# Kernel optimization log

Hardware: AMD Instinct MI355X
Metric: run time of the kernel (lower is better)

Reference implementation:

```python
import jax, jax.numpy as jnp
import numpy as np

EMB = 1024
HEAD = 64

def setup_inputs() -> dict:
    key = jax.random.key(0)
    ks = jax.random.split(key, 7)
    s = 1.0 / np.sqrt(EMB)
    X = jax.random.normal(ks[0], (4, 4096, EMB), dtype=jnp.float32)
    Wk = jax.random.uniform(ks[1], (EMB, HEAD), jnp.float32, -s, s)
    bk = jax.random.uniform(ks[2], (HEAD,), jnp.float32, -s, s)
    Wq = jax.random.uniform(ks[3], (EMB, HEAD), jnp.float32, -s, s)
    bq = jax.random.uniform(ks[4], (HEAD,), jnp.float32, -s, s)
    Wv = jax.random.uniform(ks[5], (EMB, HEAD), jnp.float32, -s, s)
    bv = jax.random.uniform(ks[6], (HEAD,), jnp.float32, -s, s)
    return {"X": X, "Wk": Wk, "bk": bk, "Wq": Wq, "bq": bq, "Wv": Wv, "bv": bv}

def reference(X, Wk, bk, Wq, bq, Wv, bv):
    # X: [B, S, E]; projections -> [B, S, H]
    k = X @ Wk + bk
    q = X @ Wq + bq
    v = X @ Wv + bv
    S = X.shape[1]
    scale = 1.0 / np.sqrt(HEAD).astype(np.float32)
    scores = jnp.einsum('bqh,bkh->bqk', q, k) * scale  # [B, S, S]
    causal = jnp.tril(jnp.ones((S, S), dtype=bool))
    scores = jnp.where(causal, scores, -jnp.inf)
    probs = jax.nn.softmax(scores, axis=-1)
    return jnp.einsum('bqk,bkh->bqh', probs, v)
```

## Files before the change

### kernel.cpp

```cpp
#include <hip/hip_runtime.h>

#define S_LEN 4096
#define EMBD  1024
#define HEADD 64

typedef __bf16 bf16x8 __attribute__((ext_vector_type(8)));
typedef float  f32x4  __attribute__((ext_vector_type(4)));

__device__ __forceinline__ unsigned short f2bf(float f) {
  union { float f; unsigned u; } x; x.f = f;
  unsigned r = x.u + 0x7FFFu + ((x.u >> 16) & 1u);
  return (unsigned short)(r >> 16);
}

__device__ __forceinline__ bf16x8 cvt8(f32x4 a, f32x4 b) {
  union { bf16x8 v; unsigned short s[8]; } u;
#pragma unroll
  for (int j = 0; j < 4; j++) { u.s[j] = f2bf(a[j]); u.s[4 + j] = f2bf(b[j]); }
  return u.v;
}

__device__ __forceinline__ unsigned fbits(float f) {
  union { float f; unsigned u; } x; x.f = f; return x.u;
}

__global__ void prep_w(const float* __restrict__ Wk, const float* __restrict__ bk,
                       const float* __restrict__ Wq, const float* __restrict__ bq,
                       const float* __restrict__ Wv, const float* __restrict__ bv,
                       unsigned short* __restrict__ wt, float* __restrict__ bias) {
  int n = blockIdx.x;
  int t = threadIdx.x;
  const float QSCALE = 0.125f * 1.44269504088896340736f;
  const float* W; const float* bsrc; int col; float s = 1.0f;
  if (n < 64)       { W = Wk; bsrc = bk; col = n; }
  else if (n < 128) { W = Wq; bsrc = bq; col = n - 64; s = QSCALE; }
  else              { W = Wv; bsrc = bv; col = n - 128; }
  for (int k = t; k < EMBD; k += 256)
    wt[n * EMBD + k] = f2bf(W[k * HEADD + col] * s);
  if (t == 0) bias[n] = bsrc[col] * s;
}

__global__ __launch_bounds__(256, 1) void proj_qkv(
    const float* __restrict__ X, const unsigned short* __restrict__ wt,
    const float* __restrict__ bias,
    unsigned short* __restrict__ qws, unsigned short* __restrict__ kws,
    unsigned short* __restrict__ vtws) {
  __shared__ unsigned short xs[64 * 256];

  const int tid = threadIdx.x;
  const int w = tid >> 6;
  const int lane = tid & 63;
  const int l15 = lane & 15, lg = lane >> 4;
  const int row0 = blockIdx.x * 64;

  const int sr = tid >> 5;
  const int sc = (tid & 31) * 8;

  const unsigned short* wp = wt + (size_t)(w * 48 + l15) * EMBD + lg * 8;

  f32x4 acc[4][3];
#pragma unroll
  for (int g = 0; g < 4; g++)
#pragma unroll
    for (int j = 0; j < 3; j++) acc[g][j] = (f32x4){0.f, 0.f, 0.f, 0.f};

  f32x4 la[8], lb[8];
#pragma unroll
  for (int it = 0; it < 8; it++) {
    const float* src = X + (size_t)(row0 + it * 8 + sr) * EMBD + sc;
    la[it] = *(const f32x4*)src;
    lb[it] = *(const f32x4*)(src + 4);
  }
#pragma unroll
  for (int it = 0; it < 8; it++) {
    const int r = it * 8 + sr;
    int soff = (r << 8) + sc;
    soff ^= (r & 7) << 3;
    *(bf16x8*)&xs[soff] = cvt8(la[it], lb[it]);
  }
  __syncthreads();

#pragma unroll
  for (int kc = 0; kc < 4; kc++) {
    if (kc + 1 < 4) {
#pragma unroll
      for (int it = 0; it < 8; it++) {
        const float* src = X + (size_t)(row0 + it * 8 + sr) * EMBD + (kc + 1) * 256 + sc;
        la[it] = *(const f32x4*)src;
        lb[it] = *(const f32x4*)(src + 4);
      }
    }
    bf16x8 wf[2][3];
#pragma unroll
    for (int j = 0; j < 3; j++)
      wf[0][j] = *(const bf16x8*)(wp + (size_t)j * 16 * EMBD + kc * 256);
#pragma unroll
    for (int ss = 0; ss < 8; ss++) {
      const int cur = ss & 1;
      if (ss + 1 < 8) {
#pragma unroll
        for (int j = 0; j < 3; j++)
          wf[cur ^ 1][j] = *(const bf16x8*)(wp + (size_t)j * 16 * EMBD + kc * 256 + (ss + 1) * 32);
      }
      const int c = ss * 32 + lg * 8;
      bf16x8 a[4];
#pragma unroll
      for (int g = 0; g < 4; g++) {
        int so = ((g * 16 + l15) << 8) + c;
        so ^= (l15 & 7) << 3;
        a[g] = *(const bf16x8*)&xs[so];
      }
#pragma unroll
      for (int j = 0; j < 3; j++)
#pragma unroll
        for (int g = 0; g < 4; g++)
          acc[g][j] = __builtin_amdgcn_mfma_f32_16x16x32_bf16(a[g], wf[cur][j], acc[g][j], 0, 0, 0);
    }
    __syncthreads();
    if (kc + 1 < 4) {
#pragma unroll
      for (int it = 0; it < 8; it++) {
        const int r = it * 8 + sr;
        int soff = (r << 8) + sc;
        soff ^= (r & 7) << 3;
        *(bf16x8*)&xs[soff] = cvt8(la[it], lb[it]);
      }
      __syncthreads();
    }
  }

#pragma unroll
  for (int g = 0; g < 4; g++) {
    const int crow0 = row0 + g * 16 + lg * 4;
#pragma unroll
    for (int j = 0; j < 3; j++) {
      const int nf = w * 3 + j;
      const int n = nf * 16 + l15;
      const float bs = bias[n];
      if (nf < 8) {
        unsigned short* dst = (nf < 4) ? kws : qws;
        const int nn = n & 63;
#pragma unroll
        for (int i = 0; i < 4; i++)
          dst[(size_t)(crow0 + i) * HEADD + nn] = f2bf(acc[g][j][i] + bs);
      } else {
        const int d = n - 128;
        const int bb = crow0 >> 12, sr2 = crow0 & 4095;
        union { unsigned long long pk; unsigned short s[4]; } u;
#pragma unroll
        for (int i = 0; i < 4; i++) u.s[i] = f2bf(acc[g][j][i] + bs);
        *(unsigned long long*)&vtws[((size_t)bb * HEADD + d) * S_LEN + sr2] = u.pk;
      }
    }
  }
}

__global__ __launch_bounds__(512, 2) void attn(
    const unsigned short* __restrict__ qws,
    const unsigned short* __restrict__ kws,
    const unsigned short* __restrict__ vtws,
    unsigned short* __restrict__ pO,
    float* __restrict__ pmv, float* __restrict__ plv) {
  __shared__ uint4 kvb[2][1024];
  __shared__ unsigned short pbl[8][16][72];

  const int tid = threadIdx.x;
  const int w = tid >> 6;
  const int lane = tid & 63;
  const int l15 = lane & 15, lg = lane >> 4;
  const int srow = tid >> 3;
  const int scol = (tid & 7) * 8;
  const int soff = ((srow * 128 + (tid & 7) * 16)) ^ ((srow & 7) << 4);

  const int id = blockIdx.x;
  const int b = id & 3;
  const int x = (id >> 2) & 15;
  const int h = id >> 6;

  const unsigned short* kb = kws + (size_t)b * S_LEN * HEADD;
  const unsigned short* vb = vtws + (size_t)b * HEADD * S_LEN;
  const unsigned short* qp = qws + (size_t)b * S_LEN * HEADD;

#define PROC(BQ0, BQ1, O, M, LL, QB, TLX, tt)                                   \
  do {                                                                          \
    f32x4 sc[4];                                                                \
    __builtin_amdgcn_s_setprio(1);                                              \
    _Pragma("unroll")                                                           \
    for (int nf = 0; nf < 4; nf++) {                                            \
      f32x4 z = (f32x4){0.f, 0.f, 0.f, 0.f};                                    \
      z = __builtin_amdgcn_mfma_f32_16x16x32_bf16(k0[nf], BQ0, z, 0, 0, 0);     \
      sc[nf] = __builtin_amdgcn_mfma_f32_16x16x32_bf16(k1[nf], BQ1, z, 0, 0, 0);\
    }                                                                           \
    __builtin_amdgcn_s_setprio(0);                                              \
    if ((tt) == (TLX)) {                                                        \
      const int qa = (QB) + l15;                                                \
      _Pragma("unroll")                                                         \
      for (int nf = 0; nf < 4; nf++)                                            \
        _Pragma("unroll")                                                       \
        for (int i = 0; i < 4; i++)                                             \
          if ((tt) * 64 + nf * 16 + lg * 4 + i > qa) sc[nf][i] = -1.0e30f;      \
    }                                                                           \
    float pm = sc[0][0];                                                        \
    _Pragma("unroll")                                                           \
    for (int nf = 0; nf < 4; nf++)                                              \
      _Pragma("unroll")                                                         \
      for (int i = 0; i < 4; i++) pm = fmaxf(pm, sc[nf][i]);                    \
    if (!__all(pm <= M + 8.0f)) {                                               \
      float mx = fmaxf(pm, __shfl_xor(pm, 16));                                 \
      mx = fmaxf(mx, __shfl_xor(mx, 32));                                       \
      const float mn = fmaxf(M, mx);                                            \
      const float al = __builtin_amdgcn_exp2f(M - mn);                          \
      M = mn;                                                                   \
      LL *= al;                                                                 \
      float alr[4];                                                             \
      _Pragma("unroll")                                                         \
      for (int i = 0; i < 4; i++) alr[i] = __shfl(al, lg * 4 + i);              \
      _Pragma("unroll")                                                         \
      for (int nd = 0; nd < 4; nd++)                                            \
        _Pragma("unroll")                                                       \
        for (int i = 0; i < 4; i++) O[nd][i] *= alr[i];                         \
    }                                                                           \
    _Pragma("unroll")                                                           \
    for (int nf = 0; nf < 4; nf++) {                                            \
      f32x4 p;                                                                  \
      _Pragma("unroll")                                                         \
      for (int i = 0; i < 4; i++) p[i] = __builtin_amdgcn_exp2f(sc[nf][i] - M); \
      LL += p[0] + p[1] + p[2] + p[3];                                          \
      unsigned lo_ = __builtin_amdgcn_perm(fbits(p[1]) + 0x8000u,               \
                                           fbits(p[0]) + 0x8000u, 0x07060302u); \
      unsigned hi_ = __builtin_amdgcn_perm(fbits(p[3]) + 0x8000u,               \
                                           fbits(p[2]) + 0x8000u, 0x07060302u); \
      uint2 pk_; pk_.x = lo_; pk_.y = hi_;                                      \
      *(uint2*)&pbl[w][l15][nf * 16 + lg * 4] = pk_;                            \
    }                                                                           \
    const bf16x8 ap0 = *(const bf16x8*)&pbl[w][l15][lg * 8];                    \
    const bf16x8 ap1 = *(const bf16x8*)&pbl[w][l15][32 + lg * 8];               \
    __builtin_amdgcn_s_setprio(1);                                              \
    _Pragma("unroll")                                                           \
    for (int nd = 0; nd < 4; nd++) {                                            \
      f32x4 oo = __builtin_amdgcn_mfma_f32_16x16x32_bf16(ap0, v0[nd], O[nd], 0, 0, 0); \
      O[nd] = __builtin_amdgcn_mfma_f32_16x16x32_bf16(ap1, v1[nd], oo, 0, 0, 0);\
    }                                                                           \
    __builtin_amdgcn_s_setprio(0);                                              \
  } while (0)

#define LOADG(tt)                                                               \
  do {                                                                          \
    kreg = *(const uint4*)(kb + ((size_t)(tt) * 64 + srow) * HEADD + scol);     \
    vreg = *(const uint4*)(vb + (size_t)srow * S_LEN + (tt) * 64 + scol);       \
  } while (0)

#define WRITEL(bf)                                                              \
  do {                                                                          \
    unsigned char* d_ = (unsigned char*)kvb[bf];                                \
    *(uint4*)&d_[soff] = kreg;                                                  \
    *(uint4*)&d_[8192 + soff] = vreg;                                           \
  } while (0)

#pragma unroll 1
  for (int ph = 0; ph < 2; ph++) {
    const int P = ph ? x : 31 - x;
    const int tlP = 2 * P + 1;
    const int tlw = 2 * P + (w >> 2);
    const int qb = P * 128 + w * 16;

    const unsigned short* qptr = qp + (size_t)(qb + l15) * HEADD + lg * 8;
    const bf16x8 bq0 = *(const bf16x8*)qptr;
    const bf16x8 bq1 = *(const bf16x8*)(qptr + 32);

    f32x4 o[4];
#pragma unroll
    for (int nd = 0; nd < 4; nd++) o[nd] = (f32x4){0.f, 0.f, 0.f, 0.f};
    float m = -3.0e38f, l = 0.f;

    int t = h;
    if (t <= tlP) {
      uint4 kreg, vreg;
      LOADG(t);
      __syncthreads();
      WRITEL(0);
      __syncthreads();
      int cur = 0;
#pragma unroll 1
      while (true) {
        const int tn = t + 8;
        const bool hn = tn <= tlP;
        if (hn) LOADG(tn);
        if (t <= tlw) {
          bf16x8 k0[4], k1[4], v0[4], v1[4];
          const unsigned char* base = (const unsigned char*)kvb[cur];
#pragma unroll
          for (int nf = 0; nf < 4; nf++) {
            const int r = nf * 16 + l15;
            const int sw = (l15 & 7) << 4;
            const int b0 = (r * 128 + lg * 16) ^ sw;
            const int b1 = (r * 128 + 64 + lg * 16) ^ sw;
            k0[nf] = *(const bf16x8*)&base[b0];
            k1[nf] = *(const bf16x8*)&base[b1];
            v0[nf] = *(const bf16x8*)&base[8192 + b0];
            v1[nf] = *(const bf16x8*)&base[8192 + b1];
          }
          PROC(bq0, bq1, o, m, l, qb, tlw, t);
        }
        if (!hn) break;
        WRITEL(cur ^ 1);
        __syncthreads();
        cur ^= 1;
        t = tn;
      }
    }

    l += __shfl_xor(l, 16);
    l += __shfl_xor(l, 32);
    const size_t pbase = (size_t)(h * 4 + b) * S_LEN + qb;
    if (lane < 16) { pmv[pbase + lane] = m; plv[pbase + lane] = l; }
#pragma unroll
    for (int nd = 0; nd < 4; nd++)
#pragma unroll
      for (int i = 0; i < 4; i++)
        pO[(pbase + lg * 4 + i) * 64 + nd * 16 + l15] = f2bf(o[nd][i]);
  }
#undef PROC
#undef LOADG
#undef WRITEL
}

__global__ __launch_bounds__(256) void merge_attn(
    const unsigned short* __restrict__ pO,
    const float* __restrict__ pmv, const float* __restrict__ plv,
    float* __restrict__ out) {
  const int row = blockIdx.x * 64 + (threadIdx.x >> 2);
  const int q = threadIdx.x & 3;
  float mh[8], lh[8];
  float M = -3.0e38f;
#pragma unroll
  for (int hh = 0; hh < 8; hh++) {
    mh[hh] = pmv[hh * 16384 + row];
    lh[hh] = plv[hh * 16384 + row];
    M = fmaxf(M, mh[hh]);
  }
  float Lt = 0.f, a[8];
#pragma unroll
  for (int hh = 0; hh < 8; hh++) {
    a[hh] = __builtin_amdgcn_exp2f(mh[hh] - M);
    Lt += a[hh] * lh[hh];
  }
  const float iL = 1.0f / Lt;
  float acc[16];
#pragma unroll
  for (int c = 0; c < 16; c++) acc[c] = 0.f;
#pragma unroll
  for (int hh = 0; hh < 8; hh++) {
    const unsigned short* src = pO + ((size_t)hh * 16384 + row) * 64 + q * 16;
    const uint4 u0 = *(const uint4*)(src);
    const uint4 u1 = *(const uint4*)(src + 8);
    const unsigned* uu0 = (const unsigned*)&u0;
    const unsigned* uu1 = (const unsigned*)&u1;
#pragma unroll
    for (int j = 0; j < 4; j++) {
      union { unsigned u; float f; } e0, e1, e2, e3;
      e0.u = uu0[j] << 16;  e1.u = uu0[j] & 0xffff0000u;
      e2.u = uu1[j] << 16;  e3.u = uu1[j] & 0xffff0000u;
      acc[j * 2 + 0] += e0.f * a[hh];
      acc[j * 2 + 1] += e1.f * a[hh];
      acc[8 + j * 2 + 0] += e2.f * a[hh];
      acc[8 + j * 2 + 1] += e3.f * a[hh];
    }
  }
  float* dst = out + (size_t)row * 64 + q * 16;
#pragma unroll
  for (int c = 0; c < 16; c++) dst[c] = acc[c] * iL;
}

extern "C" void kernel_launch(void* const* d_in, const int* in_sizes, int n_in,
                              void* d_out, int out_size, void* d_ws, size_t ws_size,
                              hipStream_t stream) {
  const float* X  = (const float*)d_in[0];
  const float* Wk = (const float*)d_in[1];
  const float* bk = (const float*)d_in[2];
  const float* Wq = (const float*)d_in[3];
  const float* bq = (const float*)d_in[4];
  const float* Wv = (const float*)d_in[5];
  const float* bv = (const float*)d_in[6];
  float* out = (float*)d_out;

  char* ws = (char*)d_ws;
  unsigned short* kws  = (unsigned short*)(ws);
  unsigned short* qws  = (unsigned short*)(ws + (2u << 20));
  unsigned short* vtws = (unsigned short*)(ws + (4u << 20));
  unsigned short* wt   = (unsigned short*)(ws + (6u << 20));
  float*          bias = (float*)(ws + (6u << 20) + (512u << 10));
  unsigned short* pO   = (unsigned short*)(ws + (8u << 20));
  float*          pmv  = (float*)(ws + (24u << 20));
  float*          plv  = (float*)(ws + (25u << 20));

  prep_w<<<dim3(192), dim3(256), 0, stream>>>(Wk, bk, Wq, bq, Wv, bv, wt, bias);
  proj_qkv<<<dim3(256), dim3(256), 0, stream>>>(X, wt, bias, qws, kws, vtws);
  attn<<<dim3(512), dim3(512), 0, stream>>>(qws, kws, vtws, pO, pmv, plv);
  merge_attn<<<dim3(256), dim3(256), 0, stream>>>(pO, pmv, plv, out);
}
```

Baseline: 66.26 us.

## Process both paired query blocks in one pass over shared K/V tiles

Replaces the two sequential phases (high and low query block) with a single loop over K/V tiles, where each staged LDS tile is consumed by both query blocks. This avoids loading the K/V tiles for the low block a second time from global memory and staging them in LDS again, and it removes one set of barriers and phase setup. The cost is double the accumulator and Q register state per thread, which can raise register pressure and lower occupancy. LDS fragments are also re-read for each block.

```diff
diff --git a/kernel.cpp b/kernel.cpp
--- a/kernel.cpp
+++ b/kernel.cpp
@@ -181,8 +181,40 @@
   const unsigned short* vb = vtws + (size_t)b * HEADD * S_LEN;
   const unsigned short* qp = qws + (size_t)b * S_LEN * HEADD;
 
-#define PROC(BQ0, BQ1, O, M, LL, QB, TLX, tt)                                   \
+  const int PH = 31 - x, PL = x;
+  const int tlPH = 2 * PH + 1;
+  const int tlwH = 2 * PH + (w >> 2);
+  const int tlwL = 2 * PL + (w >> 2);
+  const int qbH = PH * 128 + w * 16;
+  const int qbL = PL * 128 + w * 16;
+
+  const unsigned short* qH = qp + (size_t)(qbH + l15) * HEADD + lg * 8;
+  const unsigned short* qL = qp + (size_t)(qbL + l15) * HEADD + lg * 8;
+  const bf16x8 bqH0 = *(const bf16x8*)qH, bqH1 = *(const bf16x8*)(qH + 32);
+  const bf16x8 bqL0 = *(const bf16x8*)qL, bqL1 = *(const bf16x8*)(qL + 32);
+
+  f32x4 oH[4], oL[4];
+#pragma unroll
+  for (int nd = 0; nd < 4; nd++) {
+    oH[nd] = (f32x4){0.f, 0.f, 0.f, 0.f};
+    oL[nd] = (f32x4){0.f, 0.f, 0.f, 0.f};
+  }
+  float mH = -3.0e38f, lH = 0.f, mL = -3.0e38f, lL = 0.f;
+
+#define PROC(BQ0, BQ1, O, M, LL, QB, TLX, tt, base)                             \
   do {                                                                          \
+    bf16x8 k0[4], k1[4], v0[4], v1[4];                                          \
+    _Pragma("unroll")                                                           \
+    for (int nf = 0; nf < 4; nf++) {                                            \
+      const int r = nf * 16 + l15;                                              \
+      const int sw = (l15 & 7) << 4;                                            \
+      const int b0 = (r * 128 + lg * 16) ^ sw;                                  \
+      const int b1 = (r * 128 + 64 + lg * 16) ^ sw;                             \
+      k0[nf] = *(const bf16x8*)&base[b0];                                       \
+      k1[nf] = *(const bf16x8*)&base[b1];                                       \
+      v0[nf] = *(const bf16x8*)&base[8192 + b0];                                \
+      v1[nf] = *(const bf16x8*)&base[8192 + b1];                                \
+    }                                                                           \
     f32x4 sc[4];                                                                \
     __builtin_amdgcn_s_setprio(1);                                              \
     _Pragma("unroll")                                                           \
@@ -257,69 +289,48 @@
     *(uint4*)&d_[8192 + soff] = vreg;                                           \
   } while (0)
 
+  {
+    uint4 kreg, vreg;
+    int t = h;
+    LOADG(t);
+    WRITEL(0);
+    __syncthreads();
+    int cur = 0;
 #pragma unroll 1
-  for (int ph = 0; ph < 2; ph++) {
-    const int P = ph ? x : 31 - x;
-    const int tlP = 2 * P + 1;
-    const int tlw = 2 * P + (w >> 2);
-    const int qb = P * 128 + w * 16;
-
-    const unsigned short* qptr = qp + (size_t)(qb + l15) * HEADD + lg * 8;
-    const bf16x8 bq0 = *(const bf16x8*)qptr;
-    const bf16x8 bq1 = *(const bf16x8*)(qptr + 32);
-
-    f32x4 o[4];
-#pragma unroll
-    for (int nd = 0; nd < 4; nd++) o[nd] = (f32x4){0.f, 0.f, 0.f, 0.f};
-    float m = -3.0e38f, l = 0.f;
-
-    int t = h;
-    if (t <= tlP) {
-      uint4 kreg, vreg;
-      LOADG(t);
+    while (true) {
+      const int tn = t + 8;
+      const bool hn = tn <= tlPH;
+      if (hn) LOADG(tn);
+      {
+        const unsigned char* base = (const unsigned char*)kvb[cur];
+        if (t <= tlwH) PROC(bqH0, bqH1, oH, mH, lH, qbH, tlwH, t, base);
+        if (t <= tlwL) PROC(bqL0, bqL1, oL, mL, lL, qbL, tlwL, t, base);
+      }
+      if (!hn) break;
+      WRITEL(cur ^ 1);
       __syncthreads();
-      WRITEL(0);
-      __syncthreads();
-      int cur = 0;
-#pragma unroll 1
-      while (true) {
-        const int tn = t + 8;
-        const bool hn = tn <= tlP;
-        if (hn) LOADG(tn);
-        if (t <= tlw) {
-          bf16x8 k0[4], k1[4], v0[4], v1[4];
-          const unsigned char* base = (const unsigned char*)kvb[cur];
-#pragma unroll
-          for (int nf = 0; nf < 4; nf++) {
-            const int r = nf * 16 + l15;
-            const int sw = (l15 & 7) << 4;
-            const int b0 = (r * 128 + lg * 16) ^ sw;
-            const int b1 = (r * 128 + 64 + lg * 16) ^ sw;
-            k0[nf] = *(const bf16x8*)&base[b0];
-            k1[nf] = *(const bf16x8*)&base[b1];
-            v0[nf] = *(const bf16x8*)&base[8192 + b0];
-            v1[nf] = *(const bf16x8*)&base[8192 + b1];
-          }
-          PROC(bq0, bq1, o, m, l, qb, tlw, t);
-        }
-        if (!hn) break;
-        WRITEL(cur ^ 1);
-        __syncthreads();
-        cur ^= 1;
-        t = tn;
-      }
-    }
-
-    l += __shfl_xor(l, 16);
-    l += __shfl_xor(l, 32);
-    const size_t pbase = (size_t)(h * 4 + b) * S_LEN + qb;
-    if (lane < 16) { pmv[pbase + lane] = m; plv[pbase + lane] = l; }
-#pragma unroll
-    for (int nd = 0; nd < 4; nd++)
-#pragma unroll
-      for (int i = 0; i < 4; i++)
-        pO[(pbase + lg * 4 + i) * 64 + nd * 16 + l15] = f2bf(o[nd][i]);
-  }
+      cur ^= 1;
+      t = tn;
+    }
+  }
+
+  lH += __shfl_xor(lH, 16);
+  lH += __shfl_xor(lH, 32);
+  lL += __shfl_xor(lL, 16);
+  lL += __shfl_xor(lL, 32);
+  const size_t pbH = (size_t)(h * 4 + b) * S_LEN + qbH;
+  const size_t pbL = (size_t)(h * 4 + b) * S_LEN + qbL;
+  if (lane < 16) {
+    pmv[pbH + lane] = mH; plv[pbH + lane] = lH;
+    pmv[pbL + lane] = mL; plv[pbL + lane] = lL;
+  }
+#pragma unroll
+  for (int nd = 0; nd < 4; nd++)
+#pragma unroll
+    for (int i = 0; i < 4; i++) {
+      pO[(pbH + lg * 4 + i) * 64 + nd * 16 + l15] = f2bf(oH[nd][i]);
+      pO[(pbL + lg * 4 + i) * 64 + nd * 16 + l15] = f2bf(oL[nd][i]);
+    }
 #undef PROC
 #undef LOADG
 #undef WRITEL
```

After: 65.63 us. Within noise of the previous version (-1.0%).
